# Optimization experiments

Measured on AMD Instinct MI355X. Metric: run time of the kernel, lower is better.

## Reference

```python
import jax, jax.numpy as jnp
import numpy as np

N = 50000          # nodes
E = 800000         # edges (avg in-degree 16)
IN_FEATS = 256
H = 4              # num_heads
D = 32             # out_feats per head
NEG_SLOPE = 0.2


def setup_inputs() -> dict:
    key = jax.random.key(0)
    k1, k2, k3, k4, k5, k6 = jax.random.split(key, 6)
    feat = jax.random.normal(k1, (N, IN_FEATS), dtype=jnp.float32)
    src = jax.random.randint(k2, (E,), 0, N, dtype=jnp.int32)
    dst = jax.random.randint(k3, (E,), 0, N, dtype=jnp.int32)
    # parameters (xavier-ish scale)
    W = jax.random.normal(k4, (IN_FEATS, H * D), dtype=jnp.float32) * (2.0 / (IN_FEATS + H * D)) ** 0.5
    attn_l = jax.random.normal(k5, (H, D), dtype=jnp.float32) * 0.1
    attn_r = jax.random.normal(k6, (H, D), dtype=jnp.float32) * 0.1
    bias = jnp.zeros((H * D,), dtype=jnp.float32)
    return {"feat": feat, "src": src, "dst": dst, "W": W,
            "attn_l": attn_l, "attn_r": attn_r, "bias": bias}


def reference(feat, src, dst, W, attn_l, attn_r, bias):
    # dense projection: [N, H, D]
    ft = (feat @ W).reshape(N, H, D)
    # per-node attention logits: [N, H]
    el = jnp.einsum('nhd,hd->nh', ft, attn_l)
    er = jnp.einsum('nhd,hd->nh', ft, attn_r)
    # SDDMM u_add_v + leaky relu: per-edge scores [E, H]
    e = jax.nn.leaky_relu(el[src] + er[dst], negative_slope=NEG_SLOPE)
    # edge softmax over incoming edges of each dst node (segment softmax)
    m = jax.ops.segment_max(e, dst, num_segments=N)          # [N, H], -inf for empty
    e_exp = jnp.exp(e - m[dst])                               # [E, H]
    s = jax.ops.segment_sum(e_exp, dst, num_segments=N)       # [N, H]
    a = e_exp / s[dst]                                        # [E, H]
    # SpMM u_mul_e: weighted aggregation to dst nodes
    rst = jax.ops.segment_sum(ft[src] * a[:, :, None], dst, num_segments=N)  # [N, H, D]
    rst = rst + bias.reshape(1, H, D)
    return rst
```

## Files before the change

kernel.cpp:

```cpp
#include <hip/hip_runtime.h>
#include <hip/hip_bf16.h>
#include <math.h>

#define N_NODES 50000
#define N_EDGES 800000
#define IN_F 256
#define HD 128
#define NHEAD 4
#define NB_SCAN 196
#define GBM 64

typedef __attribute__((ext_vector_type(8))) short bf16x8;
typedef __attribute__((ext_vector_type(4))) float f32x4;

__device__ __forceinline__ float lrelu(float x){ return x > 0.f ? x : 0.2f * x; }

__device__ __forceinline__ unsigned short f32_to_bf16_rn(float x){
    union { float f; unsigned int u; } v; v.f = x;
    unsigned int r = v.u + 0x7FFFu + ((v.u >> 16) & 1u);
    return (unsigned short)(r >> 16);
}
__device__ __forceinline__ float bf16_to_f32(unsigned short h){
    union { unsigned int u; float f; } v; v.u = ((unsigned int)h) << 16;
    return v.f;
}
__device__ __forceinline__ float bflo(unsigned int u){
    union { unsigned int x; float f; } v; v.x = u << 16; return v.f;
}
__device__ __forceinline__ float bfhi(unsigned int u){
    union { unsigned int x; float f; } v; v.x = u & 0xFFFF0000u; return v.f;
}

__global__ void zero_ints(int* __restrict__ p, int n){
    int i = blockIdx.x * blockDim.x + threadIdx.x;
    if (i < n) p[i] = 0;
}

__global__ __launch_bounds__(256) void wsplit_kernel(const float* __restrict__ W,
                                                     unsigned short* __restrict__ Wt_hi,
                                                     unsigned short* __restrict__ Wt_lo){
    int gid = blockIdx.x * 256 + threadIdx.x;
    int n = gid >> 8;
    int k = gid & 255;
    float x = W[(size_t)k * HD + n];
    unsigned short h = f32_to_bf16_rn(x);
    float r = x - bf16_to_f32(h);
    unsigned short l = f32_to_bf16_rn(r);
    Wt_hi[gid] = h;
    Wt_lo[gid] = l;
}

__global__ __launch_bounds__(256, 4) void gemm_kernel(const float* __restrict__ feat,
                                                      const unsigned short* __restrict__ Wt_hi,
                                                      const unsigned short* __restrict__ Wt_lo,
                                                      const float* __restrict__ attn_l,
                                                      const float* __restrict__ attn_r,
                                                      unsigned short* __restrict__ ftb,
                                                      float* __restrict__ el,
                                                      float* __restrict__ er){
    __shared__ unsigned short Bh[2][8][64][8];
    __shared__ unsigned short Bl[2][8][64][8];

    const int tid  = threadIdx.x;
    const int lane = tid & 63;
    const int wv   = tid >> 6;
    const int r    = lane & 15;
    const int g    = lane >> 4;
    const int arow = blockIdx.x * GBM + wv * 16 + r;
    const bool rowok = (arow < N_NODES);
    const float* arp = feat + (size_t)arow * IN_F + g * 8;

    f32x4 acc[8];
#pragma unroll
    for (int j = 0; j < 8; ++j) acc[j] = (f32x4){0.f, 0.f, 0.f, 0.f};

    for (int kc = 0; kc < 4; ++kc){
        const int k0 = kc * 64;
#pragma unroll
        for (int i = 0; i < 4; ++i){
            int u  = tid * 4 + i;
            int l2 = u & 63;
            int fn = (u >> 6) & 7;
            int kb = u >> 9;
            int nn = fn * 16 + (l2 & 15);
            int kk = k0 + kb * 32 + (l2 >> 4) * 8;
            *(uint4*)(&Bh[kb][fn][l2][0]) = *(const uint4*)(Wt_hi + nn * 256 + kk);
            *(uint4*)(&Bl[kb][fn][l2][0]) = *(const uint4*)(Wt_lo + nn * 256 + kk);
        }
        __syncthreads();
#pragma unroll
        for (int kb = 0; kb < 2; ++kb){
            float4 v0 = make_float4(0.f, 0.f, 0.f, 0.f), v1 = v0;
            if (rowok){
                const float* fp = arp + k0 + kb * 32;
                v0 = *(const float4*)(fp);
                v1 = *(const float4*)(fp + 4);
            }
            float av[8] = {v0.x, v0.y, v0.z, v0.w, v1.x, v1.y, v1.z, v1.w};
            bf16x8 ah, al;
#pragma unroll
            for (int j = 0; j < 8; ++j){
                unsigned short h = f32_to_bf16_rn(av[j]);
                ah[j] = (short)h;
                al[j] = (short)f32_to_bf16_rn(av[j] - bf16_to_f32(h));
            }
#pragma unroll
            for (int nf = 0; nf < 8; ++nf){
                bf16x8 bh = *(const bf16x8*)(&Bh[kb][nf][lane][0]);
                bf16x8 bl = *(const bf16x8*)(&Bl[kb][nf][lane][0]);
                acc[nf] = __builtin_amdgcn_mfma_f32_16x16x32_bf16(ah, bh, acc[nf], 0, 0, 0);
                acc[nf] = __builtin_amdgcn_mfma_f32_16x16x32_bf16(ah, bl, acc[nf], 0, 0, 0);
                acc[nf] = __builtin_amdgcn_mfma_f32_16x16x32_bf16(al, bh, acc[nf], 0, 0, 0);
            }
        }
        __syncthreads();
    }
    float alv[8], arv[8];
#pragma unroll
    for (int nf = 0; nf < 8; ++nf){
        alv[nf] = attn_l[r + nf * 16];
        arv[nf] = attn_r[r + nf * 16];
    }
    const int g4 = g * 4;
#pragma unroll
    for (int rg = 0; rg < 4; ++rg){
        int gr = blockIdx.x * GBM + wv * 16 + g4 + rg;
        if (gr < N_NODES){
            unsigned short* op = ftb + (size_t)gr * HD + r;
#pragma unroll
            for (int nf = 0; nf < 8; ++nf) op[nf * 16] = f32_to_bf16_rn(acc[nf][rg]);
        }
        float pl0 = acc[0][rg] * alv[0] + acc[1][rg] * alv[1];
        float pl1 = acc[2][rg] * alv[2] + acc[3][rg] * alv[3];
        float pl2 = acc[4][rg] * alv[4] + acc[5][rg] * alv[5];
        float pl3 = acc[6][rg] * alv[6] + acc[7][rg] * alv[7];
        float pr0 = acc[0][rg] * arv[0] + acc[1][rg] * arv[1];
        float pr1 = acc[2][rg] * arv[2] + acc[3][rg] * arv[3];
        float pr2 = acc[4][rg] * arv[4] + acc[5][rg] * arv[5];
        float pr3 = acc[6][rg] * arv[6] + acc[7][rg] * arv[7];
#pragma unroll
        for (int m = 1; m <= 8; m <<= 1){
            pl0 += __shfl_xor(pl0, m, 64); pl1 += __shfl_xor(pl1, m, 64);
            pl2 += __shfl_xor(pl2, m, 64); pl3 += __shfl_xor(pl3, m, 64);
            pr0 += __shfl_xor(pr0, m, 64); pr1 += __shfl_xor(pr1, m, 64);
            pr2 += __shfl_xor(pr2, m, 64); pr3 += __shfl_xor(pr3, m, 64);
        }
        if (r == 0 && gr < N_NODES){
            *(float4*)(el + (size_t)gr * NHEAD) = make_float4(pl0, pl1, pl2, pl3);
            *(float4*)(er + (size_t)gr * NHEAD) = make_float4(pr0, pr1, pr2, pr3);
        }
    }
}

__global__ void degree_kernel(const int* __restrict__ dst, int* __restrict__ deg,
                              int* __restrict__ rank){
    int e = blockIdx.x * blockDim.x + threadIdx.x;
    if (e < N_EDGES) rank[e] = atomicAdd(&deg[dst[e]], 1);
}

__global__ __launch_bounds__(256) void scan_part(const int* __restrict__ deg,
                                                 int* __restrict__ row_off,
                                                 int* __restrict__ blk_sums){
    __shared__ int lds[256];
    int tid = threadIdx.x;
    int i = blockIdx.x * 256 + tid;
    int v = (i < N_NODES) ? deg[i] : 0;
    int x = v;
    lds[tid] = x;
    __syncthreads();
    for (int off = 1; off < 256; off <<= 1){
        int t = (tid >= off) ? lds[tid - off] : 0;
        __syncthreads();
        x += t;
        lds[tid] = x;
        __syncthreads();
    }
    if (i < N_NODES) row_off[i] = x - v;
    if (tid == 255) blk_sums[blockIdx.x] = x;
}

__global__ __launch_bounds__(256) void scan_mid(int* __restrict__ blk_sums,
                                                int* __restrict__ blk_off){
    __shared__ int lds[256];
    int tid = threadIdx.x;
    int v = (tid < NB_SCAN) ? blk_sums[tid] : 0;
    int x = v;
    lds[tid] = x;
    __syncthreads();
    for (int off = 1; off < 256; off <<= 1){
        int t = (tid >= off) ? lds[tid - off] : 0;
        __syncthreads();
        x += t;
        lds[tid] = x;
        __syncthreads();
    }
    blk_off[tid] = x - v;
}

__global__ __launch_bounds__(256) void scan_add(int* __restrict__ row_off,
                                                const int* __restrict__ blk_off){
    int i = blockIdx.x * 256 + threadIdx.x;
    if (i < N_NODES) row_off[i] += blk_off[blockIdx.x];
    if (blockIdx.x == 0 && threadIdx.x == 0) row_off[N_NODES] = N_EDGES;
}

__global__ void scatter_kernel(const int* __restrict__ src, const int* __restrict__ dst,
                               const int* __restrict__ rank, const int* __restrict__ row_off,
                               int* __restrict__ csr_src){
    int e = blockIdx.x * blockDim.x + threadIdx.x;
    if (e >= N_EDGES) return;
    csr_src[row_off[dst[e]] + rank[e]] = src[e];
}

__global__ __launch_bounds__(256) void aggregate_kernel(const unsigned short* __restrict__ ftb,
                                                        const int* __restrict__ csr_src,
                                                        const float* __restrict__ el,
                                                        const float* __restrict__ er,
                                                        const int* __restrict__ row_off,
                                                        const float* __restrict__ bias,
                                                        float* __restrict__ out){
    __shared__ float lw[4][64][4];
    __shared__ int   ls[4][64];

    const int wv   = threadIdx.x >> 6;
    const int n    = blockIdx.x * 4 + wv;
    const int lane = threadIdx.x & 63;
    const int g    = lane >> 4;
    const int l    = lane & 15;
    const int h    = l >> 2;
    const int beg  = row_off[n], end = row_off[n + 1];
    const float4 ern = *(const float4*)(er + (size_t)n * NHEAD);

    float a[8];
#pragma unroll
    for (int k = 0; k < 8; ++k) a[k] = 0.f;
    float wsum = 0.f;

    for (int base = beg; base < end; base += 64){
        int cnt = end - base; if (cnt > 64) cnt = 64;
        float4 w4 = make_float4(0.f, 0.f, 0.f, 0.f);
        int s_l = 0;
        if (lane < cnt){
            s_l = csr_src[base + lane];
            float4 elv = *(const float4*)(el + (size_t)s_l * NHEAD);
            w4.x = __expf(lrelu(elv.x + ern.x));
            w4.y = __expf(lrelu(elv.y + ern.y));
            w4.z = __expf(lrelu(elv.z + ern.z));
            w4.w = __expf(lrelu(elv.w + ern.w));
        }
        ls[wv][lane] = s_l;
        *(float4*)(&lw[wv][lane][0]) = w4;
        asm volatile("s_waitcnt lgkmcnt(0)" ::: "memory");
        __builtin_amdgcn_sched_barrier(0);
        for (int j0 = 0; j0 < cnt; j0 += 4){
            int j = j0 + g;
            float w = lw[wv][j][h];
            int   s = ls[wv][j];
            uint4 f = *(const uint4*)(ftb + (size_t)s * HD + 8 * l);
            a[0] += w * bflo(f.x); a[1] += w * bfhi(f.x);
            a[2] += w * bflo(f.y); a[3] += w * bfhi(f.y);
            a[4] += w * bflo(f.z); a[5] += w * bfhi(f.z);
            a[6] += w * bflo(f.w); a[7] += w * bfhi(f.w);
            wsum += w;
        }
        __builtin_amdgcn_sched_barrier(0);
    }
#pragma unroll
    for (int m = 16; m <= 32; m <<= 1){
#pragma unroll
        for (int k = 0; k < 8; ++k) a[k] += __shfl_xor(a[k], m, 64);
        wsum += __shfl_xor(wsum, m, 64);
    }
    float inv = (end > beg) ? 1.f / wsum : 0.f;
    if (g < 2){
        int col = 8 * l + 4 * g;
        float4 b4 = *(const float4*)(bias + col);
        float4 o;
        o.x = a[4 * g + 0] * inv + b4.x;
        o.y = a[4 * g + 1] * inv + b4.y;
        o.z = a[4 * g + 2] * inv + b4.z;
        o.w = a[4 * g + 3] * inv + b4.w;
        *(float4*)(out + (size_t)n * HD + col) = o;
    }
}

extern "C" void kernel_launch(void* const* d_in, const int* in_sizes, int n_in,
                              void* d_out, int out_size, void* d_ws, size_t ws_size,
                              hipStream_t stream){
    const float* feat   = (const float*)d_in[0];
    const int*   src    = (const int*)  d_in[1];
    const int*   dst    = (const int*)  d_in[2];
    const float* W      = (const float*)d_in[3];
    const float* attn_l = (const float*)d_in[4];
    const float* attn_r = (const float*)d_in[5];
    const float* bias   = (const float*)d_in[6];
    float* out = (float*)d_out;
    char*  ws  = (char*)d_ws;

    unsigned short* ftb = (unsigned short*)(ws + 0);
    float* el      = (float*)(ws + 12800000);
    float* er      = (float*)(ws + 13600000);
    int*   deg     = (int*)  (ws + 14400000);
    int*   rank    = (int*)  (ws + 14600000);
    int*   row_off = (int*)  (ws + 17800000);
    int*   csr_src = (int*)  (ws + 18000064);

    unsigned short* Wt_hi = (unsigned short*)csr_src;
    unsigned short* Wt_lo = Wt_hi + 32768;
    int* blk_sums = (int*)(((char*)csr_src) + 131072);
    int* blk_off  = blk_sums + 256;

    zero_ints<<<(N_NODES + 255) / 256, 256, 0, stream>>>(deg, N_NODES);
    wsplit_kernel<<<128, 256, 0, stream>>>(W, Wt_hi, Wt_lo);
    gemm_kernel<<<(N_NODES + GBM - 1) / GBM, 256, 0, stream>>>(feat, Wt_hi, Wt_lo,
                                                               attn_l, attn_r, ftb, el, er);
    degree_kernel<<<(N_EDGES + 255) / 256, 256, 0, stream>>>(dst, deg, rank);
    scan_part<<<NB_SCAN, 256, 0, stream>>>(deg, row_off, blk_sums);
    scan_mid<<<1, 256, 0, stream>>>(blk_sums, blk_off);
    scan_add<<<NB_SCAN, 256, 0, stream>>>(row_off, blk_off);
    scatter_kernel<<<(N_EDGES + 255) / 256, 256, 0, stream>>>(src, dst, rank, row_off, csr_src);
    aggregate_kernel<<<(N_NODES + 3) / 4, 256, 0, stream>>>(ftb, csr_src, el, er,
                                                            row_off, bias, out);
}
```

Measured before the change: 222.8 us.

## Merge prep kernels, drop LDS staging in GEMM, one node per 16-lane group in aggregate

The zero-degree and weight-split kernels are merged into a single launch to save one kernel launch. The GEMM no longer stages W in shared memory with barriers; each lane reads its bf16 weight fragments straight from global/L2 and prefetches the next feat chunk. The aggregation kernel now gives each 16-lane group its own destination node (16 nodes per block), which removes the cross-group shuffle reduction. The cost is lower parallelism per node and serial edge loops for high-degree nodes. Wt buffers are moved to their own workspace region so they no longer alias csr_src.

After: 253.3 us. 1.14x slower.

```diff
diff --git a/kernel.cpp b/kernel.cpp
--- a/kernel.cpp
+++ b/kernel.cpp
@@ -31,23 +31,24 @@
     union { unsigned int x; float f; } v; v.x = u & 0xFFFF0000u; return v.f;
 }
 
-__global__ void zero_ints(int* __restrict__ p, int n){
-    int i = blockIdx.x * blockDim.x + threadIdx.x;
-    if (i < n) p[i] = 0;
-}
-
-__global__ __launch_bounds__(256) void wsplit_kernel(const float* __restrict__ W,
-                                                     unsigned short* __restrict__ Wt_hi,
-                                                     unsigned short* __restrict__ Wt_lo){
-    int gid = blockIdx.x * 256 + threadIdx.x;
-    int n = gid >> 8;
-    int k = gid & 255;
-    float x = W[(size_t)k * HD + n];
-    unsigned short h = f32_to_bf16_rn(x);
-    float r = x - bf16_to_f32(h);
-    unsigned short l = f32_to_bf16_rn(r);
-    Wt_hi[gid] = h;
-    Wt_lo[gid] = l;
+__global__ __launch_bounds__(256) void prep_kernel(const float* __restrict__ W,
+                                                   unsigned short* __restrict__ Wt_hi,
+                                                   unsigned short* __restrict__ Wt_lo,
+                                                   int* __restrict__ deg){
+    int b = blockIdx.x;
+    if (b < NB_SCAN){
+        int i = b * 256 + threadIdx.x;
+        if (i < N_NODES) deg[i] = 0;
+    } else {
+        int gid = (b - NB_SCAN) * 256 + threadIdx.x;
+        int n = gid >> 8;
+        int k = gid & 255;
+        float x = W[(size_t)k * HD + n];
+        unsigned short h = f32_to_bf16_rn(x);
+        float r = x - bf16_to_f32(h);
+        Wt_hi[gid] = h;
+        Wt_lo[gid] = f32_to_bf16_rn(r);
+    }
 }
 
 __global__ __launch_bounds__(256, 4) void gemm_kernel(const float* __restrict__ feat,
@@ -58,9 +59,6 @@
                                                       unsigned short* __restrict__ ftb,
                                                       float* __restrict__ el,
                                                       float* __restrict__ er){
-    __shared__ unsigned short Bh[2][8][64][8];
-    __shared__ unsigned short Bl[2][8][64][8];
-
     const int tid  = threadIdx.x;
     const int lane = tid & 63;
     const int wv   = tid >> 6;
@@ -69,51 +67,42 @@
     const int arow = blockIdx.x * GBM + wv * 16 + r;
     const bool rowok = (arow < N_NODES);
     const float* arp = feat + (size_t)arow * IN_F + g * 8;
+    const unsigned short* bhp = Wt_hi + r * 256 + g * 8;
+    const unsigned short* blp = Wt_lo + r * 256 + g * 8;
 
     f32x4 acc[8];
 #pragma unroll
     for (int j = 0; j < 8; ++j) acc[j] = (f32x4){0.f, 0.f, 0.f, 0.f};
 
-    for (int kc = 0; kc < 4; ++kc){
-        const int k0 = kc * 64;
-#pragma unroll
-        for (int i = 0; i < 4; ++i){
-            int u  = tid * 4 + i;
-            int l2 = u & 63;
-            int fn = (u >> 6) & 7;
-            int kb = u >> 9;
-            int nn = fn * 16 + (l2 & 15);
-            int kk = k0 + kb * 32 + (l2 >> 4) * 8;
-            *(uint4*)(&Bh[kb][fn][l2][0]) = *(const uint4*)(Wt_hi + nn * 256 + kk);
-            *(uint4*)(&Bl[kb][fn][l2][0]) = *(const uint4*)(Wt_lo + nn * 256 + kk);
-        }
-        __syncthreads();
-#pragma unroll
-        for (int kb = 0; kb < 2; ++kb){
-            float4 v0 = make_float4(0.f, 0.f, 0.f, 0.f), v1 = v0;
-            if (rowok){
-                const float* fp = arp + k0 + kb * 32;
-                v0 = *(const float4*)(fp);
-                v1 = *(const float4*)(fp + 4);
-            }
-            float av[8] = {v0.x, v0.y, v0.z, v0.w, v1.x, v1.y, v1.z, v1.w};
-            bf16x8 ah, al;
-#pragma unroll
-            for (int j = 0; j < 8; ++j){
-                unsigned short h = f32_to_bf16_rn(av[j]);
-                ah[j] = (short)h;
-                al[j] = (short)f32_to_bf16_rn(av[j] - bf16_to_f32(h));
-            }
-#pragma unroll
-            for (int nf = 0; nf < 8; ++nf){
-                bf16x8 bh = *(const bf16x8*)(&Bh[kb][nf][lane][0]);
-                bf16x8 bl = *(const bf16x8*)(&Bl[kb][nf][lane][0]);
-                acc[nf] = __builtin_amdgcn_mfma_f32_16x16x32_bf16(ah, bh, acc[nf], 0, 0, 0);
-                acc[nf] = __builtin_amdgcn_mfma_f32_16x16x32_bf16(ah, bl, acc[nf], 0, 0, 0);
-                acc[nf] = __builtin_amdgcn_mfma_f32_16x16x32_bf16(al, bh, acc[nf], 0, 0, 0);
-            }
-        }
-        __syncthreads();
+    float4 a0 = make_float4(0.f,0.f,0.f,0.f), a1 = a0;
+    if (rowok){ a0 = *(const float4*)(arp); a1 = *(const float4*)(arp + 4); }
+
+#pragma unroll
+    for (int t = 0; t < 8; ++t){
+        float4 n0 = make_float4(0.f,0.f,0.f,0.f), n1 = n0;
+        if (t < 7 && rowok){
+            n0 = *(const float4*)(arp + (t + 1) * 32);
+            n1 = *(const float4*)(arp + (t + 1) * 32 + 4);
+        }
+        float av[8] = {a0.x, a0.y, a0.z, a0.w, a1.x, a1.y, a1.z, a1.w};
+        bf16x8 ah, al;
+#pragma unroll
+        for (int j = 0; j < 8; ++j){
+            unsigned short h = f32_to_bf16_rn(av[j]);
+            ah[j] = (short)h;
+            al[j] = (short)f32_to_bf16_rn(av[j] - bf16_to_f32(h));
+        }
+        const unsigned short* bh_t = bhp + t * 32;
+        const unsigned short* bl_t = blp + t * 32;
+#pragma unroll
+        for (int nf = 0; nf < 8; ++nf){
+            bf16x8 bh = *(const bf16x8*)(bh_t + nf * 4096);
+            bf16x8 bl = *(const bf16x8*)(bl_t + nf * 4096);
+            acc[nf] = __builtin_amdgcn_mfma_f32_16x16x32_bf16(ah, bh, acc[nf], 0, 0, 0);
+            acc[nf] = __builtin_amdgcn_mfma_f32_16x16x32_bf16(ah, bl, acc[nf], 0, 0, 0);
+            acc[nf] = __builtin_amdgcn_mfma_f32_16x16x32_bf16(al, bh, acc[nf], 0, 0, 0);
+        }
+        a0 = n0; a1 = n1;
     }
     float alv[8], arv[8];
 #pragma unroll
@@ -219,15 +208,15 @@
                                                         const int* __restrict__ row_off,
                                                         const float* __restrict__ bias,
                                                         float* __restrict__ out){
-    __shared__ float lw[4][64][4];
-    __shared__ int   ls[4][64];
+    __shared__ float lw[4][4][16][4];
+    __shared__ int   ls[4][4][16];
 
     const int wv   = threadIdx.x >> 6;
-    const int n    = blockIdx.x * 4 + wv;
     const int lane = threadIdx.x & 63;
-    const int g    = lane >> 4;
+    const int grp  = lane >> 4;
     const int l    = lane & 15;
     const int h    = l >> 2;
+    const int n    = blockIdx.x * 16 + wv * 4 + grp;
     const int beg  = row_off[n], end = row_off[n + 1];
     const float4 ern = *(const float4*)(er + (size_t)n * NHEAD);
 
@@ -236,26 +225,24 @@
     for (int k = 0; k < 8; ++k) a[k] = 0.f;
     float wsum = 0.f;
 
-    for (int base = beg; base < end; base += 64){
-        int cnt = end - base; if (cnt > 64) cnt = 64;
-        float4 w4 = make_float4(0.f, 0.f, 0.f, 0.f);
-        int s_l = 0;
-        if (lane < cnt){
-            s_l = csr_src[base + lane];
+    for (int base = beg; base < end; base += 16){
+        int cnt = end - base; if (cnt > 16) cnt = 16;
+        if (l < cnt){
+            int s_l = csr_src[base + l];
             float4 elv = *(const float4*)(el + (size_t)s_l * NHEAD);
+            float4 w4;
             w4.x = __expf(lrelu(elv.x + ern.x));
             w4.y = __expf(lrelu(elv.y + ern.y));
             w4.z = __expf(lrelu(elv.z + ern.z));
             w4.w = __expf(lrelu(elv.w + ern.w));
-        }
-        ls[wv][lane] = s_l;
-        *(float4*)(&lw[wv][lane][0]) = w4;
+            ls[wv][grp][l] = s_l;
+            *(float4*)(&lw[wv][grp][l][0]) = w4;
+        }
         asm volatile("s_waitcnt lgkmcnt(0)" ::: "memory");
         __builtin_amdgcn_sched_barrier(0);
-        for (int j0 = 0; j0 < cnt; j0 += 4){
-            int j = j0 + g;
-            float w = lw[wv][j][h];
-            int   s = ls[wv][j];
+        for (int j = 0; j < cnt; ++j){
+            float w = lw[wv][grp][j][h];
+            int   s = ls[wv][grp][j];
             uint4 f = *(const uint4*)(ftb + (size_t)s * HD + 8 * l);
             a[0] += w * bflo(f.x); a[1] += w * bfhi(f.x);
             a[2] += w * bflo(f.y); a[3] += w * bfhi(f.y);
@@ -265,23 +252,16 @@
         }
         __builtin_amdgcn_sched_barrier(0);
     }
-#pragma unroll
-    for (int m = 16; m <= 32; m <<= 1){
-#pragma unroll
-        for (int k = 0; k < 8; ++k) a[k] += __shfl_xor(a[k], m, 64);
-        wsum += __shfl_xor(wsum, m, 64);
-    }
     float inv = (end > beg) ? 1.f / wsum : 0.f;
-    if (g < 2){
-        int col = 8 * l + 4 * g;
-        float4 b4 = *(const float4*)(bias + col);
-        float4 o;
-        o.x = a[4 * g + 0] * inv + b4.x;
-        o.y = a[4 * g + 1] * inv + b4.y;
-        o.z = a[4 * g + 2] * inv + b4.z;
-        o.w = a[4 * g + 3] * inv + b4.w;
-        *(float4*)(out + (size_t)n * HD + col) = o;
-    }
+    float4 b0 = *(const float4*)(bias + 8 * l);
+    float4 b1 = *(const float4*)(bias + 8 * l + 4);
+    float4 o0, o1;
+    o0.x = a[0] * inv + b0.x; o0.y = a[1] * inv + b0.y;
+    o0.z = a[2] * inv + b0.z; o0.w = a[3] * inv + b0.w;
+    o1.x = a[4] * inv + b1.x; o1.y = a[5] * inv + b1.y;
+    o1.z = a[6] * inv + b1.z; o1.w = a[7] * inv + b1.w;
+    *(float4*)(out + (size_t)n * HD + 8 * l)     = o0;
+    *(float4*)(out + (size_t)n * HD + 8 * l + 4) = o1;
 }
 
 extern "C" void kernel_launch(void* const* d_in, const int* in_sizes, int n_in,
@@ -304,14 +284,13 @@
     int*   rank    = (int*)  (ws + 14600000);
     int*   row_off = (int*)  (ws + 17800000);
     int*   csr_src = (int*)  (ws + 18000064);
-
-    unsigned short* Wt_hi = (unsigned short*)csr_src;
-    unsigned short* Wt_lo = Wt_hi + 32768;
-    int* blk_sums = (int*)(((char*)csr_src) + 131072);
+    unsigned short* Wt_hi = (unsigned short*)(ws + 21200064);
+    unsigned short* Wt_lo = (unsigned short*)(ws + 21265600);
+
+    int* blk_sums = (int*)csr_src;
     int* blk_off  = blk_sums + 256;
 
-    zero_ints<<<(N_NODES + 255) / 256, 256, 0, stream>>>(deg, N_NODES);
-    wsplit_kernel<<<128, 256, 0, stream>>>(W, Wt_hi, Wt_lo);
+    prep_kernel<<<NB_SCAN + 128, 256, 0, stream>>>(W, Wt_hi, Wt_lo, deg);
     gemm_kernel<<<(N_NODES + GBM - 1) / GBM, 256, 0, stream>>>(feat, Wt_hi, Wt_lo,
                                                                attn_l, attn_r, ftb, el, er);
     degree_kernel<<<(N_EDGES + 255) / 256, 256, 0, stream>>>(dst, deg, rank);
@@ -319,6 +298,6 @@
     scan_mid<<<1, 256, 0, stream>>>(blk_sums, blk_off);
     scan_add<<<NB_SCAN, 256, 0, stream>>>(row_off, blk_off);
     scatter_kernel<<<(N_EDGES + 255) / 256, 256, 0, stream>>>(src, dst, rank, row_off, csr_src);
-    aggregate_kernel<<<(N_NODES + 3) / 4, 256, 0, stream>>>(ftb, csr_src, el, er,
-                                                            row_off, bias, out);
-}
+    aggregate_kernel<<<N_NODES / 16, 256, 0, stream>>>(ftb, csr_src, el, er,
+                                                       row_off, bias, out);
+}
```
